# Optimization experiments

Hardware: AMD Instinct MI355X
Metric: run time of the kernel (lower is better)

## Reference

```python
import jax, jax.numpy as jnp
import numpy as np

B, T, E = 2, 2048, 4096
HQ, HKV = 32, 8
D = E // HQ          # 128 head dim
G = HQ // HKV        # 4 groups


def _apply_rope(x, fr):
    # x: [B,H,T,D]; fr: [T, D/2, 2] (cos, sin)
    x = x.reshape(*x.shape[:-1], -1, 2)
    c, s = fr[..., 0], fr[..., 1]
    y = jnp.stack([x[..., 0] * c - x[..., 1] * s,
                   x[..., 1] * c + x[..., 0] * s], axis=-1)
    return y.reshape(*y.shape[:-2], -1)


def setup_inputs() -> dict:
    key = jax.random.key(0)
    ks = jax.random.split(key, 8)
    query = jax.random.normal(ks[0], (B, T, E), jnp.float32)
    kin = jax.random.normal(ks[1], (B, T, E), jnp.float32)
    vin = jax.random.normal(ks[2], (B, T, E), jnp.float32)
    s = 1.0 / np.sqrt(E)
    Wq = jax.random.normal(ks[3], (E, E), jnp.float32) * s
    Wk = jax.random.normal(ks[4], (HKV * D, E), jnp.float32) * s
    Wv = jax.random.normal(ks[5], (HKV * D, E), jnp.float32) * s
    Wo = jax.random.normal(ks[6], (E, E), jnp.float32) * s
    bq = jnp.zeros((E,), jnp.float32)
    bk = jnp.zeros((HKV * D,), jnp.float32)
    bv = jnp.zeros((HKV * D,), jnp.float32)
    bo = jnp.zeros((E,), jnp.float32)
    # standard RoPE table: [T, D/2, 2] = (cos, sin)
    inv_freq = 1.0 / (10000.0 ** (np.arange(0, D, 2, dtype=np.float32) / D))
    ang = np.outer(np.arange(T, dtype=np.float32), inv_freq)  # [T, D/2]
    freqs_cis_real_and_imag = jnp.asarray(
        np.stack([np.cos(ang), np.sin(ang)], axis=-1), jnp.float32)
    mask = jnp.tril(jnp.ones((1, 1, T, T), jnp.int32))  # causal
    return {"query": query, "key": kin, "value": vin,
            "freqs_cis_real_and_imag": freqs_cis_real_and_imag, "mask": mask,
            "Wq": Wq, "bq": bq, "Wk": Wk, "bk": bk,
            "Wv": Wv, "bv": bv, "Wo": Wo, "bo": bo}


def reference(query, key, value, freqs_cis_real_and_imag, mask,
              Wq, bq, Wk, bk, Wv, bv, Wo, bo):
    Bsz, Tlen, _ = query.shape
    Q = (query @ Wq.T + bq).reshape(Bsz, Tlen, HQ, D).transpose(0, 2, 1, 3)
    K = (key @ Wk.T + bk).reshape(Bsz, Tlen, HKV, D).transpose(0, 2, 1, 3)
    V = (value @ Wv.T + bv).reshape(Bsz, Tlen, HKV, D).transpose(0, 2, 1, 3)
    # GQA: expand kv heads to query heads (repeat_interleave on head dim)
    K = jnp.repeat(K, G, axis=1)
    V = jnp.repeat(V, G, axis=1)
    fr = freqs_cis_real_and_imag[:Tlen]
    Q = _apply_rope(Q, fr)
    K = _apply_rope(K, fr)
    score = jnp.einsum('bhqd,bhkd->bhqk', Q, K) / jnp.sqrt(jnp.float32(D))
    score = jnp.where(mask == 0, -jnp.inf, score)
    w = jax.nn.softmax(score, axis=-1)
    y = jnp.einsum('bhqk,bhkd->bhqd', w, V)
    y = y.transpose(0, 2, 1, 3).reshape(Bsz, Tlen, HQ * D)
    return y @ Wo.T + bo  # dropout: eval mode (identity)
```

## Files before the change

### kernel.cpp

```cpp
#include <hip/hip_runtime.h>
#include <hip/hip_bf16.h>

typedef __attribute__((ext_vector_type(4))) float f32x4;
typedef __attribute__((ext_vector_type(8))) short bf16x8;
typedef __attribute__((ext_vector_type(4))) short bf16x4;

#define MFMA16(a,b,c) __builtin_amdgcn_mfma_f32_16x16x32_bf16(a,b,c,0,0,0)
#define GLLDS16(g, l) __builtin_amdgcn_global_load_lds( \
    (const __attribute__((address_space(1))) unsigned int*)(g), \
    (__attribute__((address_space(3))) unsigned int*)(l), 16, 0, 0)

constexpr int BATCH = 2, SEQ = 2048, EMB = 4096;
constexpr int NHQ = 32, NHKV = 8, HD = 128, GRP = 4;

static __device__ __forceinline__ short f2bf(float f) {
    union { float f; unsigned u; } v; v.f = f;
    unsigned r = v.u + 0x7fff + ((v.u >> 16) & 1);
    return (short)(r >> 16);
}
static __device__ __forceinline__ bf16x8 cvt8(f32x4 a, f32x4 b) {
    bf16x8 r;
    r[0]=f2bf(a[0]); r[1]=f2bf(a[1]); r[2]=f2bf(a[2]); r[3]=f2bf(a[3]);
    r[4]=f2bf(b[0]); r[5]=f2bf(b[1]); r[6]=f2bf(b[2]); r[7]=f2bf(b[3]);
    return r;
}

__global__ __launch_bounds__(256) void cvt_bf16(
    const float* __restrict__ src, short* __restrict__ dst, int n8)
{
    int i = blockIdx.x * blockDim.x + threadIdx.x;
    const int stride = gridDim.x * blockDim.x;
    for (; i < n8; i += stride) {
        f32x4 a = *(const f32x4*)(src + (size_t)i * 8);
        f32x4 b = *(const f32x4*)(src + (size_t)i * 8 + 4);
        *(bf16x8*)(dst + (size_t)i * 8) = cvt8(a, b);
    }
}

template<int MODE>
__global__ __launch_bounds__(256) void gemm_bt(
    const short* __restrict__ A, const short* __restrict__ W,
    const float* __restrict__ bias, const float* __restrict__ freqs,
    void* __restrict__ outv, int M, int N, int K, int NH)
{
    __shared__ short As[128][64];
    __shared__ short Bs[128][64];

    const int tid = threadIdx.x;
    const int lane = tid & 63, wave = tid >> 6;
    const int ln = lane & 15, quad = lane >> 4;
    const int wm = wave >> 1, wn = wave & 1;
    const int rowbase = blockIdx.y * 128;
    const int colbase = blockIdx.x * 128;

    f32x4 acc[4][4];
#pragma unroll
    for (int i = 0; i < 4; i++)
#pragma unroll
        for (int j = 0; j < 4; j++) acc[i][j] = (f32x4){0.f, 0.f, 0.f, 0.f};

    for (int kk = 0; kk < K; kk += 64) {
        __syncthreads();
#pragma unroll
        for (int i = 0; i < 4; ++i) {
            const int row = wave * 32 + i * 8;
            const short* g = A + (size_t)(rowbase + row + (lane >> 3)) * K + kk + (lane & 7) * 8;
            GLLDS16(g, &As[row][0]);
        }
#pragma unroll
        for (int i = 0; i < 4; ++i) {
            const int row = wave * 32 + i * 8;
            const short* g = W + (size_t)(colbase + row + (lane >> 3)) * K + kk + (lane & 7) * 8;
            GLLDS16(g, &Bs[row][0]);
        }
        __syncthreads();

#pragma unroll
        for (int kc = 0; kc < 2; ++kc) {
            bf16x8 af[4], bfr[4];
#pragma unroll
            for (int i = 0; i < 4; i++)
                af[i] = *(const bf16x8*)&As[wm * 64 + i * 16 + ln][kc * 32 + quad * 8];
#pragma unroll
            for (int i = 0; i < 4; i++)
                bfr[i] = *(const bf16x8*)&Bs[wn * 64 + i * 16 + ln][kc * 32 + quad * 8];
#pragma unroll
            for (int i = 0; i < 4; i++)
#pragma unroll
                for (int j = 0; j < 4; j++)
                    acc[i][j] = MFMA16(af[i], bfr[j], acc[i][j]);
        }
    }

#pragma unroll
    for (int i = 0; i < 4; i++) {
        const int r0 = rowbase + wm * 64 + i * 16 + quad * 4;
#pragma unroll
        for (int j = 0; j < 4; j++) {
            const int c = colbase + wn * 64 + j * 16 + ln;
            const float bv = bias[c];
            if (MODE == 0) {
                float* out = (float*)outv;
#pragma unroll
                for (int rg = 0; rg < 4; rg++)
                    out[(size_t)(r0 + rg) * N + c] = acc[i][j][rg] + bv;
            } else if (MODE == 1) {
                short* out = (short*)outv;
                const int h = c / HD, d = c % HD;
#pragma unroll
                for (int rg = 0; rg < 4; rg++) {
                    const int r = r0 + rg;
                    const int bb = r / SEQ, t = r % SEQ;
                    const float v = acc[i][j][rg] + bv;
                    const float p = __shfl_xor(v, 1);
                    const int fi = (t * (HD / 2) + (d >> 1)) * 2;
                    const float co = freqs[fi], si = freqs[fi + 1];
                    const float y = (d & 1) ? (v * co + p * si) : (v * co - p * si);
                    out[(((size_t)bb * NH + h) * SEQ + t) * HD + d] = f2bf(y);
                }
            } else {
                short* out = (short*)outv;
                const int h = c / HD, d = c % HD;
                const int bb = r0 / SEQ, t0 = r0 % SEQ;
                bf16x4 pk;
#pragma unroll
                for (int rg = 0; rg < 4; rg++) pk[rg] = f2bf(acc[i][j][rg] + bv);
                *(bf16x4*)(out + (((size_t)bb * NHKV + h) * HD + d) * SEQ + t0) = pk;
            }
        }
    }
}

__global__ __launch_bounds__(256) void attn(
    const short* __restrict__ Qr, const short* __restrict__ Kr,
    const short* __restrict__ Vt, short* __restrict__ Y)
{
    __shared__ short Ks[2][64][128];
    __shared__ short Vs[2][128][64];
    __shared__ short Ps[4][16][80];

    const int tid = threadIdx.x;
    const int lane = tid & 63, wave = tid >> 6;
    const int ln = lane & 15, quad = lane >> 4;
    const int qt = (int)gridDim.x - 1 - (int)blockIdx.x;
    const int kvh = blockIdx.y, b = blockIdx.z;
    const int h = kvh * GRP + wave;
    const int qbase = qt * 32;
    const int sx = (ln & 7) << 3;

    const short* Qh = Qr + (((size_t)b * NHQ + h) * SEQ + qbase) * HD;
    const short* Kh = Kr + ((size_t)b * NHKV + kvh) * SEQ * HD;
    const short* Vh = Vt + ((size_t)b * NHKV + kvh) * (size_t)HD * SEQ;

    auto stage = [&](int bb, int kt) {
#pragma unroll
        for (int i = 0; i < 4; ++i) {
            const int row0 = wave * 16 + i * 4;
            const int rr = row0 + (lane >> 4);
            const short* g = Kh + (size_t)(kt * 64 + rr) * HD + (((lane & 15) ^ (rr & 7)) << 3);
            GLLDS16(g, &Ks[bb][row0][0]);
        }
#pragma unroll
        for (int i = 0; i < 4; ++i) {
            const int row0 = wave * 32 + i * 8;
            const int rr = row0 + (lane >> 3);
            const short* g = Vh + (size_t)rr * SEQ + kt * 64 + (((lane & 7) ^ (lane >> 3)) << 3);
            GLLDS16(g, &Vs[bb][row0][0]);
        }
    };

    bf16x8 aQ[2][4];
#pragma unroll
    for (int mi = 0; mi < 2; mi++)
#pragma unroll
        for (int dc = 0; dc < 4; dc++)
            aQ[mi][dc] = *(const bf16x8*)(Qh + (size_t)(mi * 16 + ln) * HD + dc * 32 + quad * 8);

    f32x4 oa[2][8];
#pragma unroll
    for (int mi = 0; mi < 2; mi++)
#pragma unroll
        for (int dt = 0; dt < 8; dt++) oa[mi][dt] = (f32x4){0.f, 0.f, 0.f, 0.f};
    float mrun[2][4], lrun[2][4];
#pragma unroll
    for (int mi = 0; mi < 2; mi++)
#pragma unroll
        for (int rg = 0; rg < 4; rg++) { mrun[mi][rg] = -INFINITY; lrun[mi][rg] = 0.f; }

    const int nkt = (qbase + 95) >> 6;
    stage(0, 0);
    __syncthreads();
    int cur = 0;

    for (int kt = 0; kt < nkt; ++kt) {
        if (kt + 1 < nkt) stage(cur ^ 1, kt + 1);

#pragma unroll
        for (int mi = 0; mi < 2; mi++) {
            float s[4][4];
            __builtin_amdgcn_s_setprio(1);
#pragma unroll
            for (int nt = 0; nt < 4; nt++) {
                f32x4 sa = (f32x4){0.f, 0.f, 0.f, 0.f};
#pragma unroll
                for (int dc = 0; dc < 4; dc++) {
                    bf16x8 bK = *(const bf16x8*)&Ks[cur][nt * 16 + ln][(dc * 32 + quad * 8) ^ sx];
                    sa = MFMA16(aQ[mi][dc], bK, sa);
                }
                const int kg = kt * 64 + nt * 16 + ln;
#pragma unroll
                for (int rg = 0; rg < 4; rg++) {
                    const int qg = qbase + mi * 16 + quad * 4 + rg;
                    s[nt][rg] = (kg <= qg) ? sa[rg] * 0.08838834764831845f : -INFINITY;
                }
            }
            __builtin_amdgcn_s_setprio(0);

            float mx4[4];
#pragma unroll
            for (int rg = 0; rg < 4; rg++) {
                float mx = fmaxf(fmaxf(s[0][rg], s[1][rg]), fmaxf(s[2][rg], s[3][rg]));
                mx = fmaxf(mx, __shfl_xor(mx, 1));
                mx = fmaxf(mx, __shfl_xor(mx, 2));
                mx = fmaxf(mx, __shfl_xor(mx, 4));
                mx = fmaxf(mx, __shfl_xor(mx, 8));
                mx4[rg] = mx;
            }
            bool ok = (mx4[0] <= mrun[mi][0] + 8.f) & (mx4[1] <= mrun[mi][1] + 8.f) &
                      (mx4[2] <= mrun[mi][2] + 8.f) & (mx4[3] <= mrun[mi][3] + 8.f);
            if (!__all(ok)) {
#pragma unroll
                for (int rg = 0; rg < 4; rg++) {
                    const float mnew = fmaxf(mrun[mi][rg], mx4[rg]);
                    const float a = __expf(mrun[mi][rg] - mnew);
                    mrun[mi][rg] = mnew;
                    lrun[mi][rg] *= a;
                    mx4[rg] = a;
                }
#pragma unroll
                for (int dt = 0; dt < 8; dt++)
#pragma unroll
                    for (int rg = 0; rg < 4; rg++) oa[mi][dt][rg] *= mx4[rg];
            }
#pragma unroll
            for (int rg = 0; rg < 4; rg++) {
                float rs = 0.f;
#pragma unroll
                for (int nt = 0; nt < 4; nt++) {
                    const float p = __expf(s[nt][rg] - mrun[mi][rg]);
                    s[nt][rg] = p; rs += p;
                }
                rs += __shfl_xor(rs, 1); rs += __shfl_xor(rs, 2);
                rs += __shfl_xor(rs, 4); rs += __shfl_xor(rs, 8);
                lrun[mi][rg] += rs;
            }
#pragma unroll
            for (int nt = 0; nt < 4; nt++)
#pragma unroll
                for (int rg = 0; rg < 4; rg++)
                    Ps[wave][quad * 4 + rg][nt * 16 + ln] = f2bf(s[nt][rg]);
            __builtin_amdgcn_s_setprio(1);
#pragma unroll
            for (int kc = 0; kc < 2; kc++) {
                bf16x8 aP = *(const bf16x8*)&Ps[wave][ln][kc * 32 + quad * 8];
#pragma unroll
                for (int dt = 0; dt < 8; dt++) {
                    bf16x8 bV = *(const bf16x8*)&Vs[cur][dt * 16 + ln][(kc * 32 + quad * 8) ^ sx];
                    oa[mi][dt] = MFMA16(aP, bV, oa[mi][dt]);
                }
            }
            __builtin_amdgcn_s_setprio(0);
        }

        __syncthreads();
        cur ^= 1;
    }

#pragma unroll
    for (int mi = 0; mi < 2; mi++) {
#pragma unroll
        for (int rg = 0; rg < 4; rg++) {
            const float inv = 1.f / lrun[mi][rg];
            const int t = qbase + mi * 16 + quad * 4 + rg;
            const size_t rowoff = ((size_t)b * SEQ + t) * EMB + h * HD;
#pragma unroll
            for (int dt = 0; dt < 8; dt++)
                Y[rowoff + dt * 16 + ln] = f2bf(oa[mi][dt][rg] * inv);
        }
    }
}

extern "C" void kernel_launch(void* const* d_in, const int* in_sizes, int n_in,
                              void* d_out, int out_size, void* d_ws, size_t ws_size,
                              hipStream_t stream) {
    const float* q  = (const float*)d_in[0];
    const float* k  = (const float*)d_in[1];
    const float* v  = (const float*)d_in[2];
    const float* fr = (const float*)d_in[3];
    const float* Wq = (const float*)d_in[5];
    const float* bq = (const float*)d_in[6];
    const float* Wk = (const float*)d_in[7];
    const float* bk = (const float*)d_in[8];
    const float* Wv = (const float*)d_in[9];
    const float* bv = (const float*)d_in[10];
    const float* Wo = (const float*)d_in[11];
    const float* bo = (const float*)d_in[12];

    char* ws = (char*)d_ws;
    short* Qr = (short*)(ws);
    short* Kr = (short*)(ws + 33554432);
    short* Vt = (short*)(ws + 41943040);
    short* Yb = (short*)(ws + 50331648);
    short* Wb = (short*)(ws + 83886080);
    float* out = (float*)d_out;

    const int M = BATCH * SEQ;
    dim3 blk(256);
    const int big8 = EMB * EMB / 8, small8 = NHKV * HD * EMB / 8, act8 = M * EMB / 8;

    cvt_bf16<<<1024, blk, 0, stream>>>(Wq, Wb, big8);
    cvt_bf16<<<1024, blk, 0, stream>>>(q, Yb, act8);
    gemm_bt<1><<<dim3(EMB / 128, M / 128), blk, 0, stream>>>(Yb, Wb, bq, fr, Qr, M, EMB, EMB, NHQ);
    cvt_bf16<<<1024, blk, 0, stream>>>(Wk, Wb, small8);
    cvt_bf16<<<1024, blk, 0, stream>>>(k, Yb, act8);
    gemm_bt<1><<<dim3((NHKV * HD) / 128, M / 128), blk, 0, stream>>>(Yb, Wb, bk, fr, Kr, M, NHKV * HD, EMB, NHKV);
    cvt_bf16<<<1024, blk, 0, stream>>>(Wv, Wb, small8);
    cvt_bf16<<<1024, blk, 0, stream>>>(v, Yb, act8);
    gemm_bt<2><<<dim3((NHKV * HD) / 128, M / 128), blk, 0, stream>>>(Yb, Wb, bv, nullptr, Vt, M, NHKV * HD, EMB, NHKV);
    attn<<<dim3(SEQ / 32, NHKV, BATCH), blk, 0, stream>>>(Qr, Kr, Vt, Yb);
    cvt_bf16<<<1024, blk, 0, stream>>>(Wo, Wb, big8);
    gemm_bt<0><<<dim3(EMB / 128, M / 128), blk, 0, stream>>>(Yb, Wb, bo, nullptr, out, M, EMB, EMB, 0);
}
```

Baseline: 1.343 ms.

## Batch K/V projections into one launch and single-buffer attention tiles

K and V projection GEMMs are merged into a single kernel launch that uses a z grid dimension to select K or V. Their inputs are converted to bf16 into separate workspace regions, using the Q buffer as scratch for V. The K/V GEMMs had only 8x32 blocks each, so the merge is meant to fill more CUs per launch and save a launch. Separately, attention drops the double-buffered K/V LDS staging for a single buffer with sync-stage-sync-compute and asks for 3 blocks per CU via launch bounds. This trades load/compute overlap for higher occupancy.

```diff
diff --git a/kernel.cpp b/kernel.cpp
--- a/kernel.cpp
+++ b/kernel.cpp
@@ -37,40 +37,28 @@
     }
 }
 
-template<int MODE>
-__global__ __launch_bounds__(256) void gemm_bt(
+
+struct GemmCtx {
+    int lane, wave, ln, quad, wm, wn, rowbase, colbase;
+};
+
+static __device__ __forceinline__ void gemm_mainloop(
+    short (&As)[128][64], short (&Bs)[128][64],
     const short* __restrict__ A, const short* __restrict__ W,
-    const float* __restrict__ bias, const float* __restrict__ freqs,
-    void* __restrict__ outv, int M, int N, int K, int NH)
-{
-    __shared__ short As[128][64];
-    __shared__ short Bs[128][64];
-
-    const int tid = threadIdx.x;
-    const int lane = tid & 63, wave = tid >> 6;
-    const int ln = lane & 15, quad = lane >> 4;
-    const int wm = wave >> 1, wn = wave & 1;
-    const int rowbase = blockIdx.y * 128;
-    const int colbase = blockIdx.x * 128;
-
-    f32x4 acc[4][4];
-#pragma unroll
-    for (int i = 0; i < 4; i++)
-#pragma unroll
-        for (int j = 0; j < 4; j++) acc[i][j] = (f32x4){0.f, 0.f, 0.f, 0.f};
-
+    int K, const GemmCtx& c, f32x4 (&acc)[4][4])
+{
     for (int kk = 0; kk < K; kk += 64) {
         __syncthreads();
 #pragma unroll
         for (int i = 0; i < 4; ++i) {
-            const int row = wave * 32 + i * 8;
-            const short* g = A + (size_t)(rowbase + row + (lane >> 3)) * K + kk + (lane & 7) * 8;
+            const int row = c.wave * 32 + i * 8;
+            const short* g = A + (size_t)(c.rowbase + row + (c.lane >> 3)) * K + kk + (c.lane & 7) * 8;
             GLLDS16(g, &As[row][0]);
         }
 #pragma unroll
         for (int i = 0; i < 4; ++i) {
-            const int row = wave * 32 + i * 8;
-            const short* g = W + (size_t)(colbase + row + (lane >> 3)) * K + kk + (lane & 7) * 8;
+            const int row = c.wave * 32 + i * 8;
+            const short* g = W + (size_t)(c.colbase + row + (c.lane >> 3)) * K + kk + (c.lane & 7) * 8;
             GLLDS16(g, &Bs[row][0]);
         }
         __syncthreads();
@@ -80,10 +68,10 @@
             bf16x8 af[4], bfr[4];
 #pragma unroll
             for (int i = 0; i < 4; i++)
-                af[i] = *(const bf16x8*)&As[wm * 64 + i * 16 + ln][kc * 32 + quad * 8];
+                af[i] = *(const bf16x8*)&As[c.wm * 64 + i * 16 + c.ln][kc * 32 + c.quad * 8];
 #pragma unroll
             for (int i = 0; i < 4; i++)
-                bfr[i] = *(const bf16x8*)&Bs[wn * 64 + i * 16 + ln][kc * 32 + quad * 8];
+                bfr[i] = *(const bf16x8*)&Bs[c.wn * 64 + i * 16 + c.ln][kc * 32 + c.quad * 8];
 #pragma unroll
             for (int i = 0; i < 4; i++)
 #pragma unroll
@@ -91,22 +79,29 @@
                     acc[i][j] = MFMA16(af[i], bfr[j], acc[i][j]);
         }
     }
-
+}
+
+template<int MODE>
+static __device__ __forceinline__ void gemm_epilogue(
+    const f32x4 (&acc)[4][4], const float* __restrict__ bias,
+    const float* __restrict__ freqs, void* __restrict__ outv,
+    int N, int NH, const GemmCtx& c)
+{
 #pragma unroll
     for (int i = 0; i < 4; i++) {
-        const int r0 = rowbase + wm * 64 + i * 16 + quad * 4;
+        const int r0 = c.rowbase + c.wm * 64 + i * 16 + c.quad * 4;
 #pragma unroll
         for (int j = 0; j < 4; j++) {
-            const int c = colbase + wn * 64 + j * 16 + ln;
-            const float bv = bias[c];
+            const int col = c.colbase + c.wn * 64 + j * 16 + c.ln;
+            const float bv = bias[col];
             if (MODE == 0) {
                 float* out = (float*)outv;
 #pragma unroll
                 for (int rg = 0; rg < 4; rg++)
-                    out[(size_t)(r0 + rg) * N + c] = acc[i][j][rg] + bv;
+                    out[(size_t)(r0 + rg) * N + col] = acc[i][j][rg] + bv;
             } else if (MODE == 1) {
                 short* out = (short*)outv;
-                const int h = c / HD, d = c % HD;
+                const int h = col / HD, d = col % HD;
 #pragma unroll
                 for (int rg = 0; rg < 4; rg++) {
                     const int r = r0 + rg;
@@ -120,7 +115,7 @@
                 }
             } else {
                 short* out = (short*)outv;
-                const int h = c / HD, d = c % HD;
+                const int h = col / HD, d = col % HD;
                 const int bb = r0 / SEQ, t0 = r0 % SEQ;
                 bf16x4 pk;
 #pragma unroll
@@ -131,12 +126,69 @@
     }
 }
 
-__global__ __launch_bounds__(256) void attn(
+template<int MODE>
+__global__ __launch_bounds__(256) void gemm_bt(
+    const short* __restrict__ A, const short* __restrict__ W,
+    const float* __restrict__ bias, const float* __restrict__ freqs,
+    void* __restrict__ outv, int M, int N, int K, int NH)
+{
+    __shared__ short As[128][64];
+    __shared__ short Bs[128][64];
+    const int tid = threadIdx.x;
+    GemmCtx c;
+    c.lane = tid & 63; c.wave = tid >> 6;
+    c.ln = c.lane & 15; c.quad = c.lane >> 4;
+    c.wm = c.wave >> 1; c.wn = c.wave & 1;
+    c.rowbase = blockIdx.y * 128; c.colbase = blockIdx.x * 128;
+
+    f32x4 acc[4][4];
+#pragma unroll
+    for (int i = 0; i < 4; i++)
+#pragma unroll
+        for (int j = 0; j < 4; j++) acc[i][j] = (f32x4){0.f, 0.f, 0.f, 0.f};
+
+    gemm_mainloop(As, Bs, A, W, K, c, acc);
+    gemm_epilogue<MODE>(acc, bias, freqs, outv, N, NH, c);
+}
+
+__global__ __launch_bounds__(256) void gemm_kv(
+    const short* __restrict__ Ak, const short* __restrict__ Wkb,
+    const float* __restrict__ bk, const float* __restrict__ freqs,
+    void* __restrict__ outK,
+    const short* __restrict__ Av, const short* __restrict__ Wvb,
+    const float* __restrict__ bv, void* __restrict__ outV,
+    int M, int N, int K)
+{
+    __shared__ short As[128][64];
+    __shared__ short Bs[128][64];
+    const int tid = threadIdx.x;
+    GemmCtx c;
+    c.lane = tid & 63; c.wave = tid >> 6;
+    c.ln = c.lane & 15; c.quad = c.lane >> 4;
+    c.wm = c.wave >> 1; c.wn = c.wave & 1;
+    c.rowbase = blockIdx.y * 128; c.colbase = blockIdx.x * 128;
+    const int z = blockIdx.z;
+
+    const short* A = (z == 0) ? Ak : Av;
+    const short* W = (z == 0) ? Wkb : Wvb;
+
+    f32x4 acc[4][4];
+#pragma unroll
+    for (int i = 0; i < 4; i++)
+#pragma unroll
+        for (int j = 0; j < 4; j++) acc[i][j] = (f32x4){0.f, 0.f, 0.f, 0.f};
+
+    gemm_mainloop(As, Bs, A, W, K, c, acc);
+    if (z == 0) gemm_epilogue<1>(acc, bk, freqs, outK, N, NHKV, c);
+    else        gemm_epilogue<2>(acc, bv, nullptr, outV, N, NHKV, c);
+}
+
+__global__ __launch_bounds__(256, 3) void attn(
     const short* __restrict__ Qr, const short* __restrict__ Kr,
     const short* __restrict__ Vt, short* __restrict__ Y)
 {
-    __shared__ short Ks[2][64][128];
-    __shared__ short Vs[2][128][64];
+    __shared__ short Ks[64][128];
+    __shared__ short Vs[128][64];
     __shared__ short Ps[4][16][80];
 
     const int tid = threadIdx.x;
@@ -152,49 +204,42 @@
     const short* Kh = Kr + ((size_t)b * NHKV + kvh) * SEQ * HD;
     const short* Vh = Vt + ((size_t)b * NHKV + kvh) * (size_t)HD * SEQ;
 
-    auto stage = [&](int bb, int kt) {
+    bf16x8 aQ[2][4];
+#pragma unroll
+    for (int mi = 0; mi < 2; mi++)
+#pragma unroll
+        for (int dc = 0; dc < 4; dc++)
+            aQ[mi][dc] = *(const bf16x8*)(Qh + (size_t)(mi * 16 + ln) * HD + dc * 32 + quad * 8);
+
+    f32x4 oa[2][8];
+#pragma unroll
+    for (int mi = 0; mi < 2; mi++)
+#pragma unroll
+        for (int dt = 0; dt < 8; dt++) oa[mi][dt] = (f32x4){0.f, 0.f, 0.f, 0.f};
+    float mrun[2][4], lrun[2][4];
+#pragma unroll
+    for (int mi = 0; mi < 2; mi++)
+#pragma unroll
+        for (int rg = 0; rg < 4; rg++) { mrun[mi][rg] = -INFINITY; lrun[mi][rg] = 0.f; }
+
+    auto stage = [&](int kt) {
 #pragma unroll
         for (int i = 0; i < 4; ++i) {
             const int row0 = wave * 16 + i * 4;
             const int rr = row0 + (lane >> 4);
             const short* g = Kh + (size_t)(kt * 64 + rr) * HD + (((lane & 15) ^ (rr & 7)) << 3);
-            GLLDS16(g, &Ks[bb][row0][0]);
+            GLLDS16(g, &Ks[row0][0]);
         }
 #pragma unroll
         for (int i = 0; i < 4; ++i) {
             const int row0 = wave * 32 + i * 8;
             const int rr = row0 + (lane >> 3);
             const short* g = Vh + (size_t)rr * SEQ + kt * 64 + (((lane & 7) ^ (lane >> 3)) << 3);
-            GLLDS16(g, &Vs[bb][row0][0]);
+            GLLDS16(g, &Vs[row0][0]);
         }
     };
 
-    bf16x8 aQ[2][4];
-#pragma unroll
-    for (int mi = 0; mi < 2; mi++)
-#pragma unroll
-        for (int dc = 0; dc < 4; dc++)
-            aQ[mi][dc] = *(const bf16x8*)(Qh + (size_t)(mi * 16 + ln) * HD + dc * 32 + quad * 8);
-
-    f32x4 oa[2][8];
-#pragma unroll
-    for (int mi = 0; mi < 2; mi++)
-#pragma unroll
-        for (int dt = 0; dt < 8; dt++) oa[mi][dt] = (f32x4){0.f, 0.f, 0.f, 0.f};
-    float mrun[2][4], lrun[2][4];
-#pragma unroll
-    for (int mi = 0; mi < 2; mi++)
-#pragma unroll
-        for (int rg = 0; rg < 4; rg++) { mrun[mi][rg] = -INFINITY; lrun[mi][rg] = 0.f; }
-
-    const int nkt = (qbase + 95) >> 6;
-    stage(0, 0);
-    __syncthreads();
-    int cur = 0;
-
-    for (int kt = 0; kt < nkt; ++kt) {
-        if (kt + 1 < nkt) stage(cur ^ 1, kt + 1);
-
+    auto compute = [&](int kt) {
 #pragma unroll
         for (int mi = 0; mi < 2; mi++) {
             float s[4][4];
@@ -204,7 +249,7 @@
                 f32x4 sa = (f32x4){0.f, 0.f, 0.f, 0.f};
 #pragma unroll
                 for (int dc = 0; dc < 4; dc++) {
-                    bf16x8 bK = *(const bf16x8*)&Ks[cur][nt * 16 + ln][(dc * 32 + quad * 8) ^ sx];
+                    bf16x8 bK = *(const bf16x8*)&Ks[nt * 16 + ln][(dc * 32 + quad * 8) ^ sx];
                     sa = MFMA16(aQ[mi][dc], bK, sa);
                 }
                 const int kg = kt * 64 + nt * 16 + ln;
@@ -265,15 +310,20 @@
                 bf16x8 aP = *(const bf16x8*)&Ps[wave][ln][kc * 32 + quad * 8];
 #pragma unroll
                 for (int dt = 0; dt < 8; dt++) {
-                    bf16x8 bV = *(const bf16x8*)&Vs[cur][dt * 16 + ln][(kc * 32 + quad * 8) ^ sx];
+                    bf16x8 bV = *(const bf16x8*)&Vs[dt * 16 + ln][(kc * 32 + quad * 8) ^ sx];
                     oa[mi][dt] = MFMA16(aP, bV, oa[mi][dt]);
                 }
             }
             __builtin_amdgcn_s_setprio(0);
         }
-
+    };
+
+    const int nkt = (qbase + 95) >> 6;
+    for (int kt = 0; kt < nkt; ++kt) {
         __syncthreads();
-        cur ^= 1;
+        stage(kt);
+        __syncthreads();
+        compute(kt);
     }
 
 #pragma unroll
@@ -317,16 +367,18 @@
     const int M = BATCH * SEQ;
     dim3 blk(256);
     const int big8 = EMB * EMB / 8, small8 = NHKV * HD * EMB / 8, act8 = M * EMB / 8;
-
+    short* WbK = Wb;
+    short* WbV = Wb + (size_t)NHKV * HD * EMB;
+
+    cvt_bf16<<<1024, blk, 0, stream>>>(Wk, WbK, small8);
+    cvt_bf16<<<1024, blk, 0, stream>>>(Wv, WbV, small8);
+    cvt_bf16<<<1024, blk, 0, stream>>>(k, Yb, act8);
+    cvt_bf16<<<1024, blk, 0, stream>>>(v, Qr, act8);
+    gemm_kv<<<dim3((NHKV * HD) / 128, M / 128, 2), blk, 0, stream>>>(
+        Yb, WbK, bk, fr, Kr, Qr, WbV, bv, Vt, M, NHKV * HD, EMB);
     cvt_bf16<<<1024, blk, 0, stream>>>(Wq, Wb, big8);
     cvt_bf16<<<1024, blk, 0, stream>>>(q, Yb, act8);
     gemm_bt<1><<<dim3(EMB / 128, M / 128), blk, 0, stream>>>(Yb, Wb, bq, fr, Qr, M, EMB, EMB, NHQ);
-    cvt_bf16<<<1024, blk, 0, stream>>>(Wk, Wb, small8);
-    cvt_bf16<<<1024, blk, 0, stream>>>(k, Yb, act8);
-    gemm_bt<1><<<dim3((NHKV * HD) / 128, M / 128), blk, 0, stream>>>(Yb, Wb, bk, fr, Kr, M, NHKV * HD, EMB, NHKV);
-    cvt_bf16<<<1024, blk, 0, stream>>>(Wv, Wb, small8);
-    cvt_bf16<<<1024, blk, 0, stream>>>(v, Yb, act8);
-    gemm_bt<2><<<dim3((NHKV * HD) / 128, M / 128), blk, 0, stream>>>(Yb, Wb, bv, nullptr, Vt, M, NHKV * HD, EMB, NHKV);
     attn<<<dim3(SEQ / 32, NHKV, BATCH), blk, 0, stream>>>(Qr, Kr, Vt, Yb);
     cvt_bf16<<<1024, blk, 0, stream>>>(Wo, Wb, big8);
     gemm_bt<0><<<dim3(EMB / 128, M / 128), blk, 0, stream>>>(Yb, Wb, bo, nullptr, out, M, EMB, EMB, 0);
```

Result: slower. 1.549 ms (+15.3%).
